# Optimization experiments

Hardware: AMD Instinct MI355X
Metric: run time of the kernel (lower is better)

## Reference

```python
import math
import jax, jax.numpy as jnp
import numpy as np

N_HEADS = 8
FACTOR = 1


def setup_inputs() -> dict:
    key = jax.random.key(0)
    ks = jax.random.split(key, 8)
    B, L, D = 8, 2048, 512
    scale = 0.05
    return {
        "queries": jax.random.normal(ks[0], (B, L, D), jnp.float32),
        "keys": jax.random.normal(ks[1], (B, L, D), jnp.float32),
        "values": jax.random.normal(ks[2], (B, L, D), jnp.float32),
        "Wq": jax.random.normal(ks[3], (D, D), jnp.float32) * scale,
        "bq": jnp.zeros((D,), jnp.float32),
        "Wk": jax.random.normal(ks[4], (D, D), jnp.float32) * scale,
        "bk": jnp.zeros((D,), jnp.float32),
        "Wv": jax.random.normal(ks[5], (D, D), jnp.float32) * scale,
        "bv": jnp.zeros((D,), jnp.float32),
        "Wo": jax.random.normal(ks[6], (D, D), jnp.float32) * scale,
        "bo": jnp.zeros((D,), jnp.float32),
    }


def _autocorrelation(q, k, v):
    # q,k,v: [B, L, H, E]; L == S assumed (as built in setup_inputs)
    B, L, H, E = q.shape
    qp = jnp.transpose(q, (0, 2, 3, 1))  # [B,H,E,L]
    kp = jnp.transpose(k, (0, 2, 3, 1))
    vp = jnp.transpose(v, (0, 2, 3, 1))
    q_fft = jnp.fft.rfft(qp, axis=-1)
    k_fft = jnp.fft.rfft(kp, axis=-1)
    corr = jnp.fft.irfft(q_fft * jnp.conj(k_fft), n=L, axis=-1)  # [B,H,E,L]

    # training-path time-delay aggregation
    top_k = int(FACTOR * math.log(L))  # static python int
    mean_value = corr.mean(axis=(1, 2))  # [B, L]
    _, index = jax.lax.top_k(mean_value.mean(axis=0), top_k)  # [K] global delays
    weights = mean_value[:, index]  # [B, K]
    tmp_corr = jax.nn.softmax(weights, axis=-1)  # [B, K]
    # roll(v, -d) along last axis == gather at (t + d) mod L
    idx = (jnp.arange(L)[None, :] + index[:, None]) % L  # [K, L]
    patterns = vp[..., idx]  # [B,H,E,K,L]
    delays_agg = jnp.einsum('bhekl,bk->bhel', patterns, tmp_corr)  # [B,H,E,L]
    return jnp.transpose(delays_agg, (0, 3, 1, 2))  # [B,L,H,E]


def reference(queries, keys, values, Wq, bq, Wk, bk, Wv, bv, Wo, bo):
    B, L, Dm = queries.shape
    H = N_HEADS
    q = (queries @ Wq + bq).reshape(B, L, H, -1)
    k = (keys @ Wk + bk).reshape(B, L, H, -1)
    v = (values @ Wv + bv).reshape(B, L, H, -1)
    out = _autocorrelation(q, k, v).reshape(B, L, -1)
    return out @ Wo + bo
```

## Files before the change

kernel.cpp:

```cpp
#include <hip/hip_runtime.h>
#include <stdint.h>

#define BATCH 8
#define L_SEQ 2048
#define D_MODEL 512
#define TOPK 7
#define BM 128
#define BN 128
#define BK 32
#define LT 136

typedef _Float16 f16x8 __attribute__((ext_vector_type(8)));
typedef __attribute__((ext_vector_type(4))) float f32x4;
typedef unsigned short u16;
typedef unsigned int u32;

__device__ __forceinline__ u16 f2h(float f) {
    union { _Float16 h; u16 u; } v; v.h = (_Float16)f; return v.u;
}

__device__ __forceinline__ void load_lds16(const u16* g, u16* l) {
    __builtin_amdgcn_global_load_lds(
        (const __attribute__((address_space(1))) u32*)(g),
        (__attribute__((address_space(3))) u32*)(l), 16, 0, 0);
}


__global__ __launch_bounds__(256, 3) void gemm_qkv(
    const float* __restrict__ Xq, const float* __restrict__ Xk, const float* __restrict__ Xv,
    const u16* __restrict__ Wqt, const u16* __restrict__ Wkt, const u16* __restrict__ Wvt,
    const float* __restrict__ bq, const float* __restrict__ bk, const float* __restrict__ bv,
    u16* __restrict__ QT, u16* __restrict__ KT, u16* __restrict__ Vout)
{
    __shared__ __align__(16) u16 smem[2 * BM * 32 + 2 * BN * BK];
    u16* lT = smem;
    u16* lBb = smem + 2 * BM * 32;

    const int tid = threadIdx.x;
    const int hw = blockIdx.x;
    const int lg = (hw & 7) * 192 + (hw >> 3);
    const int bn = lg & 3, bm = (lg >> 2) & 127, z = lg >> 9;

    const int lane = tid & 63, wave = tid >> 6;
    const int wm = wave >> 1, wn = wave & 1;
    const int l15 = lane & 15, quad = lane >> 4;

    const float* A  = (z == 0) ? Xq  : (z == 1) ? Xk  : Xv;
    const u16*   Bt = (z == 0) ? Wqt : (z == 1) ? Wkt : Wvt;
    const float* bias = (z == 0) ? bq : (z == 1) ? bk : bv;

    const int s0 = wave * 64 + lane, s1 = s0 + 256;
    const int r0 = s0 >> 2, c0 = (s0 & 3) ^ ((r0 >> 1) & 3);
    const int r1 = s1 >> 2, c1 = (s1 & 3) ^ ((r1 >> 1) & 3);
    const u16* gB0 = Bt + (long)(bn * BN + r0) * D_MODEL + c0 * 8;
    const u16* gB1 = Bt + (long)(bn * BN + r1) * D_MODEL + c1 * 8;

    int rowj[4], csj[4];
    const float* gA[4];
    #pragma unroll
    for (int j = 0; j < 4; ++j) {
        int idx = tid + j * 256;
        int row = idx >> 3, c4 = (idx & 7) * 4;
        rowj[j] = row;
        csj[j] = (((c4 >> 3) ^ (row & 3)) << 3) | (c4 & 7);
        gA[j] = A + (long)(bm * BM + row) * D_MODEL + c4;
    }

    f32x4 acc[4][4] = {};
    float4 vaA[4];

    {
        load_lds16(gB0, lBb + wave * 512);
        load_lds16(gB1, lBb + 2048 + wave * 512);
        gB0 += BK; gB1 += BK;
        #pragma unroll
        for (int j = 0; j < 4; ++j) {
            float4 va = *(const float4*)(gA[j]);
            ushort4 pa;
            pa.x = f2h(va.x); pa.y = f2h(va.y); pa.z = f2h(va.z); pa.w = f2h(va.w);
            *(ushort4*)&smem[rowj[j] * 32 + csj[j]] = pa;
        }
        #pragma unroll
        for (int j = 0; j < 4; ++j)
            vaA[j] = *(const float4*)(gA[j] + BK);
    }
    __syncthreads();

    #define QKV_FRAGS_MFMA(lAc_, lBc_)                                              \
        {                                                                           \
            f16x8 fa[4], fb[4];                                                     \
            _Pragma("unroll")                                                       \
            for (int i = 0; i < 4; ++i) {                                           \
                int r = wm * 64 + i * 16 + l15;                                     \
                fa[i] = *(const f16x8*)&(lAc_)[r * 32 + ((quad ^ (r & 3)) << 3)];   \
            }                                                                       \
            _Pragma("unroll")                                                       \
            for (int j = 0; j < 4; ++j) {                                           \
                int n = wn * 64 + j * 16 + l15;                                     \
                int cs = quad ^ ((n >> 1) & 3);                                     \
                fb[j] = *(const f16x8*)&(lBc_)[n * 32 + cs * 8];                    \
            }                                                                       \
            _Pragma("unroll")                                                       \
            for (int i = 0; i < 4; ++i)                                             \
                _Pragma("unroll")                                                   \
                for (int j = 0; j < 4; ++j)                                         \
                    acc[i][j] = __builtin_amdgcn_mfma_f32_16x16x32_f16(             \
                        fa[i], fb[j], acc[i][j], 0, 0, 0);                          \
        }

    for (int t = 0; t < 14; ++t) {
        const int cur = t & 1;
        u16* lAc = smem + cur * (BM * 32);
        u16* lBc = lBb + cur * (BN * BK);
        u16* lAn = smem + (cur ^ 1) * (BM * 32);
        u16* lBn = lBb + (cur ^ 1) * (BN * BK);

        #pragma unroll
        for (int j = 0; j < 4; ++j) {
            ushort4 pa;
            pa.x = f2h(vaA[j].x); pa.y = f2h(vaA[j].y);
            pa.z = f2h(vaA[j].z); pa.w = f2h(vaA[j].w);
            *(ushort4*)&lAn[rowj[j] * 32 + csj[j]] = pa;
        }
        __builtin_amdgcn_sched_barrier(0);
        load_lds16(gB0, lBn + wave * 512);
        load_lds16(gB1, lBn + 2048 + wave * 512);
        gB0 += BK; gB1 += BK;
        __builtin_amdgcn_sched_barrier(0);
        #pragma unroll
        for (int j = 0; j < 4; ++j)
            vaA[j] = *(const float4*)(gA[j] + (t + 2) * BK);

        QKV_FRAGS_MFMA(lAc, lBc)

        asm volatile("s_waitcnt vmcnt(4) lgkmcnt(0)" ::: "memory");
        __builtin_amdgcn_sched_barrier(0);
        __builtin_amdgcn_s_barrier();
        __builtin_amdgcn_sched_barrier(0);
    }

    {
        u16* lAc = smem;
        u16* lBc = lBb;
        u16* lAn = smem + BM * 32;
        u16* lBn = lBb + BN * BK;
        #pragma unroll
        for (int j = 0; j < 4; ++j) {
            ushort4 pa;
            pa.x = f2h(vaA[j].x); pa.y = f2h(vaA[j].y);
            pa.z = f2h(vaA[j].z); pa.w = f2h(vaA[j].w);
            *(ushort4*)&lAn[rowj[j] * 32 + csj[j]] = pa;
        }
        __builtin_amdgcn_sched_barrier(0);
        load_lds16(gB0, lBn + wave * 512);
        load_lds16(gB1, lBn + 2048 + wave * 512);

        QKV_FRAGS_MFMA(lAc, lBc)

        asm volatile("s_waitcnt vmcnt(0) lgkmcnt(0)" ::: "memory");
        __builtin_amdgcn_sched_barrier(0);
        __builtin_amdgcn_s_barrier();
        __builtin_amdgcn_sched_barrier(0);
    }

    {
        u16* lAc = smem + BM * 32;
        u16* lBc = lBb + BN * BK;
        QKV_FRAGS_MFMA(lAc, lBc)
    }
    #undef QKV_FRAGS_MFMA

    if (z < 2) {
        u16* out = (z == 0) ? QT : KT;
        const int t0 = (bm * BM) & (L_SEQ - 1);
        const int bb = (bm * BM) >> 11;
        #pragma unroll
        for (int h = 0; h < 2; ++h) {
            __syncthreads();
            if (wn == h) {
                #pragma unroll
                for (int j = 0; j < 4; ++j) {
                    int dloc = j * 16 + l15;
                    float bvv = bias[bn * BN + h * 64 + dloc];
                    #pragma unroll
                    for (int i = 0; i < 4; ++i) {
                        int trow = wm * 64 + i * 16 + quad * 4;
                        #pragma unroll
                        for (int r = 0; r < 4; ++r)
                            lT[dloc * LT + trow + r] = f2h(acc[i][j][r] + bvv);
                    }
                }
            }
            __syncthreads();
            int dloc = tid >> 2, q4 = tid & 3;
            long base = ((long)(bb * D_MODEL + bn * BN + h * 64 + dloc)) * L_SEQ + t0;
            #pragma unroll
            for (int s = 0; s < 4; ++s) {
                int c = q4 * 4 + s;
                *(uint4*)(out + base + c * 8) = *(const uint4*)&lT[dloc * LT + c * 8];
            }
        }
    } else {
        #pragma unroll
        for (int i = 0; i < 4; ++i) {
            int row = bm * BM + wm * 64 + i * 16 + quad * 4;
            #pragma unroll
            for (int j = 0; j < 4; ++j) {
                int col = bn * BN + wn * 64 + j * 16 + l15;
                float bvv = bias[col];
                #pragma unroll
                for (int r = 0; r < 4; ++r)
                    Vout[(long)(row + r) * D_MODEL + col] = f2h(acc[i][j][r] + bvv);
            }
        }
    }
}

__global__ __launch_bounds__(256, 3) void gemm_out_fused(
    const u16* __restrict__ V, const u16* __restrict__ Bt,
    const int* __restrict__ selIdx, const float* __restrict__ selW,
    const float* __restrict__ bias, float* __restrict__ Cp)
{
    __shared__ __align__(16) u16 lA[2 * BM * 32];
    __shared__ __align__(16) u16 lB[2 * BN * BK];

    const int tid = threadIdx.x;
    const int hw = blockIdx.x;
    const int lg = (hw & 7) * 64 + (hw >> 3);
    const int bn = lg & 3, bm = lg >> 2;

    const int lane = tid & 63, wave = tid >> 6;
    const int wm = wave >> 1, wn = wave & 1;
    const int l15 = lane & 15, quad = lane >> 4;

    int sik[TOPK];
    #pragma unroll
    for (int k = 0; k < TOPK; ++k) sik[k] = selIdx[k];

    const int s0 = wave * 64 + lane, s1 = s0 + 256;
    const int r0 = s0 >> 2, c0 = (s0 & 3) ^ ((r0 >> 1) & 3);
    const int r1 = s1 >> 2, c1 = (s1 & 3) ^ ((r1 >> 1) & 3);
    const u16* gB0 = Bt + (long)(bn * BN + r0) * D_MODEL + c0 * 8;
    const u16* gB1 = Bt + (long)(bn * BN + r1) * D_MODEL + c1 * 8;

    const int row_a = tid >> 2,          c8_a = (tid & 3) * 8;
    const int row_b = (tid + 256) >> 2,  c8_b = (tid & 3) * 8;
    const int csa = ((c8_a >> 3) ^ (row_a & 3)) << 3;
    const int csb = ((c8_b >> 3) ^ (row_b & 3)) << 3;
    const int gra = bm * BM + row_a, grb = bm * BM + row_b;
    const int ba = gra >> 11, la = gra & (L_SEQ - 1);
    const int bb = grb >> 11, lb = grb & (L_SEQ - 1);

    _Float16 swa[TOPK], swb[TOPK];
    #pragma unroll
    for (int k = 0; k < TOPK; ++k) {
        swa[k] = (_Float16)selW[ba * TOPK + k];
        swb[k] = (_Float16)selW[bb * TOPK + k];
    }

    union U8 { uint4 u; f16x8 h8; };

    f32x4 acc[4][4] = {};

    {
        load_lds16(gB0, lB + wave * 512);
        load_lds16(gB1, lB + 2048 + wave * 512);
        gB0 += BK; gB1 += BK;
        {
            f16x8 a = {};
            #pragma unroll
            for (int k = 0; k < TOPK; ++k) {
                int src = (la + sik[k]) & (L_SEQ - 1);
                U8 x; x.u = *(const uint4*)(V + ((long)ba * L_SEQ + src) * D_MODEL + c8_a);
                a += x.h8 * swa[k];
            }
            U8 o; o.h8 = a;
            *(uint4*)&lA[row_a * 32 + csa] = o.u;
        }
        {
            f16x8 a = {};
            #pragma unroll
            for (int k = 0; k < TOPK; ++k) {
                int src = (lb + sik[k]) & (L_SEQ - 1);
                U8 x; x.u = *(const uint4*)(V + ((long)bb * L_SEQ + src) * D_MODEL + c8_b);
                a += x.h8 * swb[k];
            }
            U8 o; o.h8 = a;
            *(uint4*)&lA[row_b * 32 + csb] = o.u;
        }
    }
    __syncthreads();

    for (int t = 0; t < 16; ++t) {
        const int cur = t & 1;
        u16* lAc = lA + cur * (BM * 32);
        u16* lBc = lB + cur * (BN * BK);
        u16* lAn = lA + (cur ^ 1) * (BM * 32);
        u16* lBn = lB + (cur ^ 1) * (BN * BK);
        const bool nx = (t < 15);
        const int k1 = (t + 1) * BK;

        U8 xv[7];
        if (nx) {
            load_lds16(gB0, lBn + wave * 512);
            load_lds16(gB1, lBn + 2048 + wave * 512);
            gB0 += BK; gB1 += BK;
            #pragma unroll
            for (int k = 0; k < TOPK; ++k) {
                int src = (la + sik[k]) & (L_SEQ - 1);
                xv[k].u = *(const uint4*)(V + ((long)ba * L_SEQ + src) * D_MODEL + k1 + c8_a);
            }
        }

        f16x8 fa[4], fb[4];
        #pragma unroll
        for (int i = 0; i < 4; ++i) {
            int r = wm * 64 + i * 16 + l15;
            fa[i] = *(const f16x8*)&lAc[r * 32 + ((quad ^ (r & 3)) << 3)];
        }
        #pragma unroll
        for (int j = 0; j < 4; ++j) {
            int n = wn * 64 + j * 16 + l15;
            int cs = quad ^ ((n >> 1) & 3);
            fb[j] = *(const f16x8*)&lBc[n * 32 + cs * 8];
        }

        #pragma unroll
        for (int i = 0; i < 2; ++i)
            #pragma unroll
            for (int j = 0; j < 4; ++j)
                acc[i][j] = __builtin_amdgcn_mfma_f32_16x16x32_f16(fa[i], fb[j], acc[i][j], 0, 0, 0);

        U8 xw[7];
        if (nx) {
            f16x8 a = {};
            #pragma unroll
            for (int k = 0; k < TOPK; ++k) a += xv[k].h8 * swa[k];
            U8 o; o.h8 = a;
            *(uint4*)&lAn[row_a * 32 + csa] = o.u;
            #pragma unroll
            for (int k = 0; k < TOPK; ++k) {
                int src = (lb + sik[k]) & (L_SEQ - 1);
                xw[k].u = *(const uint4*)(V + ((long)bb * L_SEQ + src) * D_MODEL + k1 + c8_b);
            }
        }

        #pragma unroll
        for (int i = 2; i < 4; ++i)
            #pragma unroll
            for (int j = 0; j < 4; ++j)
                acc[i][j] = __builtin_amdgcn_mfma_f32_16x16x32_f16(fa[i], fb[j], acc[i][j], 0, 0, 0);

        if (nx) {
            f16x8 a = {};
            #pragma unroll
            for (int k = 0; k < TOPK; ++k) a += xw[k].h8 * swb[k];
            U8 o; o.h8 = a;
            *(uint4*)&lAn[row_b * 32 + csb] = o.u;
        }
        __syncthreads();
    }

    #pragma unroll
    for (int i = 0; i < 4; ++i) {
        int row = bm * BM + wm * 64 + i * 16 + quad * 4;
        #pragma unroll
        for (int j = 0; j < 4; ++j) {
            int col = bn * BN + wn * 64 + j * 16 + l15;
            float bvv = bias[col];
            #pragma unroll
            for (int r = 0; r < 4; ++r)
                Cp[(long)(row + r) * D_MODEL + col] = acc[i][j][r] + bvv;
        }
    }
}

__device__ __forceinline__ void fft2048_lds2(
    float2* Z, const float2* Tw, int tid)
{
    #pragma unroll
    for (int s = 0; s < 10; s += 2) {
        #pragma unroll
        for (int u = 0; u < 2; ++u) {
            int idx = tid + u * 256;
            int d1 = 1 << s;
            int pos = idx & (d1 - 1);
            int i0 = ((idx >> s) << (s + 2)) + pos;
            float2 w1 = Tw[pos << (10 - s)];
            float2 w2 = Tw[pos << (9 - s)];
            float2 w3 = Tw[(pos + d1) << (9 - s)];
            float2 a = Z[i0];
            float2 b = Z[i0 + d1];
            float2 c = Z[i0 + 2 * d1];
            float2 d = Z[i0 + 3 * d1];
            float t1r = b.x * w1.x - b.y * w1.y, t1i = b.x * w1.y + b.y * w1.x;
            float Ar = a.x + t1r, Ai = a.y + t1i, Br = a.x - t1r, Bi = a.y - t1i;
            float t2r = d.x * w1.x - d.y * w1.y, t2i = d.x * w1.y + d.y * w1.x;
            float Cr = c.x + t2r, Ci = c.y + t2i, Dr = c.x - t2r, Di = c.y - t2i;
            float u1r = Cr * w2.x - Ci * w2.y, u1i = Cr * w2.y + Ci * w2.x;
            float u2r = Dr * w3.x - Di * w3.y, u2i = Dr * w3.y + Di * w3.x;
            float2 o;
            o.x = Ar + u1r; o.y = Ai + u1i; Z[i0]          = o;
            o.x = Ar - u1r; o.y = Ai - u1i; Z[i0 + 2 * d1] = o;
            o.x = Br + u2r; o.y = Bi + u2i; Z[i0 + d1]     = o;
            o.x = Br - u2r; o.y = Bi - u2i; Z[i0 + 3 * d1] = o;
        }
        __syncthreads();
    }
    #pragma unroll
    for (int j = 0; j < 4; ++j) {
        int idx = tid + j * 256;
        float2 w = Tw[idx];
        float2 a = Z[idx], b = Z[idx + 1024];
        float tr = b.x * w.x - b.y * w.y, ti = b.x * w.y + b.y * w.x;
        float2 o;
        o.x = a.x + tr; o.y = a.y + ti; Z[idx] = o;
        o.x = a.x - tr; o.y = a.y - ti; Z[idx + 1024] = o;
    }
    __syncthreads();
}

__global__ __launch_bounds__(256) void fft_corr_fwd(
    const u16* __restrict__ QT, const u16* __restrict__ KT, float* __restrict__ S)
{
    __shared__ float2 Z[2048];
    __shared__ float2 Tw[1024];
    const int tid = threadIdx.x;
    const int b = blockIdx.x >> 7, dg = blockIdx.x & 127;

    #pragma unroll
    for (int j = 0; j < 4; ++j) {
        int i = tid + j * 256;
        float ang = -6.28318530717958647692f * (float)i * (1.0f / 2048.0f);
        float sn, cs; __sincosf(ang, &sn, &cs);
        float2 w; w.x = cs; w.y = sn;
        Tw[i] = w;
    }

    float sr[8] = {0,0,0,0,0,0,0,0};
    float si8[8] = {0,0,0,0,0,0,0,0};

    for (int g = 0; g < 4; ++g) {
        int d = dg * 4 + g;
        const u16* qrow = QT + ((long)b * D_MODEL + d) * L_SEQ;
        const u16* krow = KT + ((long)b * D_MODEL + d) * L_SEQ;
        __syncthreads();
        union { uint4 u; _Float16 h[8]; } xq, xk;
        xq.u = *(const uint4*)(qrow + tid * 8);
        xk.u = *(const uint4*)(krow + tid * 8);
        #pragma unroll
        for (int j = 0; j < 8; ++j) {
            int t = tid * 8 + j;
            int tr = (int)(__brev((unsigned)t) >> 21);
            float2 z; z.x = (float)xq.h[j]; z.y = (float)xk.h[j];
            Z[tr] = z;
        }
        __syncthreads();
        fft2048_lds2(Z, Tw, tid);
        #pragma unroll
        for (int j = 0; j < 8; ++j) {
            int f = tid + j * 256;
            int fm = (2048 - f) & 2047;
            float2 X = Z[f], Xm = Z[fm];
            float qr = 0.5f * (X.x + Xm.x), qi = 0.5f * (X.y - Xm.y);
            float dr = X.x - Xm.x,          di = X.y + Xm.y;
            float kr = 0.5f * di,           ki = -0.5f * dr;
            sr[j]  += qr * kr + qi * ki;
            si8[j] += qi * kr - qr * ki;
        }
    }
    #pragma unroll
    for (int j = 0; j < 8; ++j) {
        int f = tid + j * 256;
        atomicAdd(&S[((long)b * 2048 + f) * 2 + 0], sr[j]);
        atomicAdd(&S[((long)b * 2048 + f) * 2 + 1], si8[j]);
    }
}

__global__ __launch_bounds__(256) void fft_corr_inv(
    const float* __restrict__ S, float* __restrict__ raw)
{
    __shared__ float2 Z[2048];
    __shared__ float2 Tw[1024];
    const int tid = threadIdx.x;
    const int b = blockIdx.x;

    #pragma unroll
    for (int j = 0; j < 4; ++j) {
        int i = tid + j * 256;
        float ang = 6.28318530717958647692f * (float)i * (1.0f / 2048.0f);
        float sn, cs; __sincosf(ang, &sn, &cs);
        float2 w; w.x = cs; w.y = sn;
        Tw[i] = w;
    }
    #pragma unroll
    for (int j = 0; j < 8; ++j) {
        int f = tid + j * 256;
        int fr = (int)(__brev((unsigned)f) >> 21);
        Z[fr] = *(const float2*)(S + ((long)b * 2048 + f) * 2);
    }
    __syncthreads();
    fft2048_lds2(Z, Tw, tid);
    #pragma unroll
    for (int j = 0; j < 8; ++j) {
        int t = tid + j * 256;
        raw[(long)b * 2048 + t] = Z[t].x * (1.0f / 2048.0f);
    }
}

__global__ __launch_bounds__(256) void transposeW4(
    const float* __restrict__ Wq, const float* __restrict__ Wk,
    const float* __restrict__ Wv, const float* __restrict__ Wo, u16* __restrict__ dstBase)
{
    __shared__ float t[32][33];
    const int z = blockIdx.z;
    const float* src = (z == 0) ? Wq : (z == 1) ? Wk : (z == 2) ? Wv : Wo;
    u16* dst = dstBase + (long)z * D_MODEL * D_MODEL;
    int tx = threadIdx.x & 31, ty = threadIdx.x >> 5;
    int c0 = blockIdx.x * 32, r0 = blockIdx.y * 32;
    #pragma unroll
    for (int r = ty; r < 32; r += 8)
        t[r][tx] = src[(long)(r0 + r) * D_MODEL + c0 + tx];
    __syncthreads();
    #pragma unroll
    for (int r = ty; r < 32; r += 8)
        dst[(long)(c0 + r) * D_MODEL + r0 + tx] = f2h(t[tx][r]);
}

__global__ __launch_bounds__(256) void select_topk(
    const float* __restrict__ raw, int* __restrict__ selIdx, float* __restrict__ selW)
{
    __shared__ float g[L_SEQ];
    __shared__ float wv[4];
    __shared__ int   wi[4];
    __shared__ int   sidx[TOPK];
    __shared__ float wbuf[BATCH][TOPK];
    int tid = threadIdx.x;
    int lane = tid & 63, wave = tid >> 6;
    for (int t = tid; t < L_SEQ; t += 256) {
        float s = 0.0f;
        #pragma unroll
        for (int b = 0; b < BATCH; ++b) s += raw[b * L_SEQ + t];
        g[t] = s;
    }
    __syncthreads();
    for (int it = 0; it < TOPK; ++it) {
        float best = -1e30f; int bi = 0x7fffffff;
        #pragma unroll
        for (int j = 0; j < 8; ++j) {
            int t = tid + j * 256;
            float v = g[t];
            if (v > best || (v == best && t < bi)) { best = v; bi = t; }
        }
        #pragma unroll
        for (int s = 32; s > 0; s >>= 1) {
            float v2 = __shfl_xor(best, s);
            int   i2 = __shfl_xor(bi, s);
            if (v2 > best || (v2 == best && i2 < bi)) { best = v2; bi = i2; }
        }
        if (lane == 0) { wv[wave] = best; wi[wave] = bi; }
        __syncthreads();
        if (tid == 0) {
            float b0 = wv[0]; int i0 = wi[0];
            #pragma unroll
            for (int w = 1; w < 4; ++w)
                if (wv[w] > b0 || (wv[w] == b0 && wi[w] < i0)) { b0 = wv[w]; i0 = wi[w]; }
            sidx[it] = i0; g[i0] = -1e30f;
        }
        __syncthreads();
    }
    if (tid < BATCH * TOPK) {
        int b = tid / TOPK, k = tid % TOPK;
        wbuf[b][k] = raw[b * L_SEQ + sidx[k]] * (1.0f / 512.0f);
    }
    __syncthreads();
    if (tid < BATCH) {
        float mx = -1e30f;
        #pragma unroll
        for (int k = 0; k < TOPK; ++k) mx = fmaxf(mx, wbuf[tid][k]);
        float e[TOPK]; float sum = 0.0f;
        #pragma unroll
        for (int k = 0; k < TOPK; ++k) { e[k] = expf(wbuf[tid][k] - mx); sum += e[k]; }
        #pragma unroll
        for (int k = 0; k < TOPK; ++k) selW[tid * TOPK + k] = e[k] / sum;
    }
    if (tid < TOPK) selIdx[tid] = sidx[tid];
}

extern "C" void kernel_launch(void* const* d_in, const int* in_sizes, int n_in,
                              void* d_out, int out_size, void* d_ws, size_t ws_size,
                              hipStream_t stream)
{
    (void)in_sizes; (void)n_in; (void)out_size; (void)ws_size;
    const float* Xq = (const float*)d_in[0];
    const float* Xk = (const float*)d_in[1];
    const float* Xv = (const float*)d_in[2];
    const float* Wq = (const float*)d_in[3];
    const float* bq = (const float*)d_in[4];
    const float* Wk = (const float*)d_in[5];
    const float* bk = (const float*)d_in[6];
    const float* Wv = (const float*)d_in[7];
    const float* bv = (const float*)d_in[8];
    const float* Wo = (const float*)d_in[9];
    const float* bo = (const float*)d_in[10];

    char* ws = (char*)d_ws;
    const long SLABH = (long)BATCH * L_SEQ * D_MODEL * sizeof(u16);
    u16* QT   = (u16*)(ws);
    u16* KT   = (u16*)(ws + SLABH);
    u16* Vf   = (u16*)(ws + 2 * SLABH);
    const long WSZ = (long)D_MODEL * D_MODEL;
    u16* Wt   = (u16*)(ws + 3 * SLABH);
    u16* Wqt = Wt + 0 * WSZ; u16* Wkt = Wt + 1 * WSZ;
    u16* Wvt = Wt + 2 * WSZ; u16* Wot = Wt + 3 * WSZ;
    float* S   = (float*)(ws + 3 * SLABH + 4 * WSZ * sizeof(u16));
    float* raw = S + (long)BATCH * L_SEQ * 2;
    int*   sIdx = (int*)(raw + (long)BATCH * L_SEQ);
    float* sW   = (float*)(sIdx + 8);

    dim3 tb(256);
    transposeW4<<<dim3(16, 16, 4), tb, 0, stream>>>(Wq, Wk, Wv, Wo, Wt);
    hipMemsetAsync(S, 0, (long)BATCH * L_SEQ * 2 * sizeof(float), stream);

    gemm_qkv<<<dim3(1536), tb, 0, stream>>>(Xq, Xk, Xv, Wqt, Wkt, Wvt, bq, bk, bv, QT, KT, Vf);

    fft_corr_fwd<<<dim3(1024), tb, 0, stream>>>(QT, KT, S);
    fft_corr_inv<<<dim3(BATCH), tb, 0, stream>>>(S, raw);
    select_topk<<<1, tb, 0, stream>>>(raw, sIdx, sW);

    gemm_out_fused<<<dim3(512), tb, 0, stream>>>(Vf, Wot, sIdx, sW, bo, (float*)d_out);
}
```

Baseline: 311.0 us.

## Fuse inverse FFT with top-k selection using linearity and direct DFT for weights

Sums the per-batch spectra before a single inverse FFT, relying on linearity, so one block computes the batch-summed correlation instead of eight separate inverse FFTs. The same block then runs the top-k selection and evaluates each batch's correlation at the chosen delays with a direct DFT sum over the spectrum, removing the separate select_topk launch and the raw buffer. The memset of S is folded into the weight-transpose kernel, so one fewer API call is made. The cost is that the fused stage runs as one serial block doing extra DFT work, where the inverse FFTs previously ran across eight blocks.

```diff
diff --git a/kernel.cpp b/kernel.cpp
--- a/kernel.cpp
+++ b/kernel.cpp
@@ -477,13 +477,19 @@
     }
 }
 
-__global__ __launch_bounds__(256) void fft_corr_inv(
-    const float* __restrict__ S, float* __restrict__ raw)
+__global__ __launch_bounds__(256) void fft_inv_topk(
+    const float* __restrict__ S, int* __restrict__ selIdx, float* __restrict__ selW)
 {
     __shared__ float2 Z[2048];
     __shared__ float2 Tw[1024];
+    __shared__ float g[L_SEQ];
+    __shared__ float wv[4];
+    __shared__ int   wi[4];
+    __shared__ int   sidx[TOPK];
+    __shared__ float wbuf[BATCH][TOPK];
+
     const int tid = threadIdx.x;
-    const int b = blockIdx.x;
+    const int lane = tid & 63, wave = tid >> 6;
 
     #pragma unroll
     for (int j = 0; j < 4; ++j) {
@@ -497,20 +503,89 @@
     for (int j = 0; j < 8; ++j) {
         int f = tid + j * 256;
         int fr = (int)(__brev((unsigned)f) >> 21);
-        Z[fr] = *(const float2*)(S + ((long)b * 2048 + f) * 2);
+        float sx = 0.f, sy = 0.f;
+        #pragma unroll
+        for (int b = 0; b < BATCH; ++b) {
+            float2 v = *(const float2*)(S + ((long)b * 2048 + f) * 2);
+            sx += v.x; sy += v.y;
+        }
+        float2 z; z.x = sx; z.y = sy;
+        Z[fr] = z;
     }
     __syncthreads();
     fft2048_lds2(Z, Tw, tid);
     #pragma unroll
     for (int j = 0; j < 8; ++j) {
         int t = tid + j * 256;
-        raw[(long)b * 2048 + t] = Z[t].x * (1.0f / 2048.0f);
-    }
+        g[t] = Z[t].x * (1.0f / 2048.0f);
+    }
+    __syncthreads();
+
+    for (int it = 0; it < TOPK; ++it) {
+        float best = -1e30f; int bi = 0x7fffffff;
+        #pragma unroll
+        for (int j = 0; j < 8; ++j) {
+            int t = tid + j * 256;
+            float v = g[t];
+            if (v > best || (v == best && t < bi)) { best = v; bi = t; }
+        }
+        #pragma unroll
+        for (int s = 32; s > 0; s >>= 1) {
+            float v2 = __shfl_xor(best, s);
+            int   i2 = __shfl_xor(bi, s);
+            if (v2 > best || (v2 == best && i2 < bi)) { best = v2; bi = i2; }
+        }
+        if (lane == 0) { wv[wave] = best; wi[wave] = bi; }
+        __syncthreads();
+        if (tid == 0) {
+            float b0 = wv[0]; int i0 = wi[0];
+            #pragma unroll
+            for (int w = 1; w < 4; ++w)
+                if (wv[w] > b0 || (wv[w] == b0 && wi[w] < i0)) { b0 = wv[w]; i0 = wi[w]; }
+            sidx[it] = i0; g[i0] = -1e30f;
+        }
+        __syncthreads();
+    }
+
+    #pragma unroll
+    for (int h = 0; h < 2; ++h) {
+        int b = wave + h * 4;
+        #pragma unroll
+        for (int k = 0; k < TOPK; ++k) {
+            int idx = sidx[k];
+            float part = 0.f;
+            for (int i = 0; i < 32; ++i) {
+                int f = lane + i * 64;
+                int m = (f * idx) & 2047;
+                float2 w2 = Tw[m & 1023];
+                float2 sv = *(const float2*)(S + ((long)b * 2048 + f) * 2);
+                float re = sv.x * w2.x - sv.y * w2.y;
+                part += (m & 1024) ? -re : re;
+            }
+            #pragma unroll
+            for (int s = 32; s > 0; s >>= 1) part += __shfl_xor(part, s);
+            if (lane == 0) wbuf[b][k] = part * (1.0f / 2048.0f) * (1.0f / 512.0f);
+        }
+    }
+    __syncthreads();
+
+    if (tid < BATCH) {
+        float mx = -1e30f;
+        #pragma unroll
+        for (int k = 0; k < TOPK; ++k) mx = fmaxf(mx, wbuf[tid][k]);
+        float e[TOPK]; float sum = 0.0f;
+        #pragma unroll
+        for (int k = 0; k < TOPK; ++k) { e[k] = expf(wbuf[tid][k] - mx); sum += e[k]; }
+        #pragma unroll
+        for (int k = 0; k < TOPK; ++k) selW[tid * TOPK + k] = e[k] / sum;
+    }
+    if (tid < TOPK) selIdx[tid] = sidx[tid];
 }
 
 __global__ __launch_bounds__(256) void transposeW4(
     const float* __restrict__ Wq, const float* __restrict__ Wk,
-    const float* __restrict__ Wv, const float* __restrict__ Wo, u16* __restrict__ dstBase)
+    const float* __restrict__ Wv, const float* __restrict__ Wo, u16* __restrict__ dstBase,
+    float* __restrict__ Sz)
 {
     __shared__ float t[32][33];
     const int z = blockIdx.z;
@@ -518,6 +593,10 @@
     u16* dst = dstBase + (long)z * D_MODEL * D_MODEL;
     int tx = threadIdx.x & 31, ty = threadIdx.x >> 5;
     int c0 = blockIdx.x * 32, r0 = blockIdx.y * 32;
+
+    const int fb = (blockIdx.z * 16 + blockIdx.y) * 16 + blockIdx.x;
+    if (threadIdx.x < 32) Sz[fb * 32 + threadIdx.x] = 0.0f;
+
     #pragma unroll
     for (int r = ty; r < 32; r += 8)
         t[r][tx] = src[(long)(r0 + r) * D_MODEL + c0 + tx];
@@ -525,66 +604,6 @@
     #pragma unroll
     for (int r = ty; r < 32; r += 8)
         dst[(long)(c0 + r) * D_MODEL + r0 + tx] = f2h(t[tx][r]);
-}
-
-__global__ __launch_bounds__(256) void select_topk(
-    const float* __restrict__ raw, int* __restrict__ selIdx, float* __restrict__ selW)
-{
-    __shared__ float g[L_SEQ];
-    __shared__ float wv[4];
-    __shared__ int   wi[4];
-    __shared__ int   sidx[TOPK];
-    __shared__ float wbuf[BATCH][TOPK];
-    int tid = threadIdx.x;
-    int lane = tid & 63, wave = tid >> 6;
-    for (int t = tid; t < L_SEQ; t += 256) {
-        float s = 0.0f;
-        #pragma unroll
-        for (int b = 0; b < BATCH; ++b) s += raw[b * L_SEQ + t];
-        g[t] = s;
-    }
-    __syncthreads();
-    for (int it = 0; it < TOPK; ++it) {
-        float best = -1e30f; int bi = 0x7fffffff;
-        #pragma unroll
-        for (int j = 0; j < 8; ++j) {
-            int t = tid + j * 256;
-            float v = g[t];
-            if (v > best || (v == best && t < bi)) { best = v; bi = t; }
-        }
-        #pragma unroll
-        for (int s = 32; s > 0; s >>= 1) {
-            float v2 = __shfl_xor(best, s);
-            int   i2 = __shfl_xor(bi, s);
-            if (v2 > best || (v2 == best && i2 < bi)) { best = v2; bi = i2; }
-        }
-        if (lane == 0) { wv[wave] = best; wi[wave] = bi; }
-        __syncthreads();
-        if (tid == 0) {
-            float b0 = wv[0]; int i0 = wi[0];
-            #pragma unroll
-            for (int w = 1; w < 4; ++w)
-                if (wv[w] > b0 || (wv[w] == b0 && wi[w] < i0)) { b0 = wv[w]; i0 = wi[w]; }
-            sidx[it] = i0; g[i0] = -1e30f;
-        }
-        __syncthreads();
-    }
-    if (tid < BATCH * TOPK) {
-        int b = tid / TOPK, k = tid % TOPK;
-        wbuf[b][k] = raw[b * L_SEQ + sidx[k]] * (1.0f / 512.0f);
-    }
-    __syncthreads();
-    if (tid < BATCH) {
-        float mx = -1e30f;
-        #pragma unroll
-        for (int k = 0; k < TOPK; ++k) mx = fmaxf(mx, wbuf[tid][k]);
-        float e[TOPK]; float sum = 0.0f;
-        #pragma unroll
-        for (int k = 0; k < TOPK; ++k) { e[k] = expf(wbuf[tid][k] - mx); sum += e[k]; }
-        #pragma unroll
-        for (int k = 0; k < TOPK; ++k) selW[tid * TOPK + k] = e[k] / sum;
-    }
-    if (tid < TOPK) selIdx[tid] = sidx[tid];
 }
 
 extern "C" void kernel_launch(void* const* d_in, const int* in_sizes, int n_in,
@@ -614,19 +633,16 @@
     u16* Wqt = Wt + 0 * WSZ; u16* Wkt = Wt + 1 * WSZ;
     u16* Wvt = Wt + 2 * WSZ; u16* Wot = Wt + 3 * WSZ;
     float* S   = (float*)(ws + 3 * SLABH + 4 * WSZ * sizeof(u16));
-    float* raw = S + (long)BATCH * L_SEQ * 2;
-    int*   sIdx = (int*)(raw + (long)BATCH * L_SEQ);
+    int*   sIdx = (int*)(S + (long)BATCH * L_SEQ * 2);
     float* sW   = (float*)(sIdx + 8);
 
     dim3 tb(256);
-    transposeW4<<<dim3(16, 16, 4), tb, 0, stream>>>(Wq, Wk, Wv, Wo, Wt);
-    hipMemsetAsync(S, 0, (long)BATCH * L_SEQ * 2 * sizeof(float), stream);
+    transposeW4<<<dim3(16, 16, 4), tb, 0, stream>>>(Wq, Wk, Wv, Wo, Wt, S);
 
     gemm_qkv<<<dim3(1536), tb, 0, stream>>>(Xq, Xk, Xv, Wqt, Wkt, Wvt, bq, bk, bv, QT, KT, Vf);
 
     fft_corr_fwd<<<dim3(1024), tb, 0, stream>>>(QT, KT, S);
-    fft_corr_inv<<<dim3(BATCH), tb, 0, stream>>>(S, raw);
-    select_topk<<<1, tb, 0, stream>>>(raw, sIdx, sW);
+    fft_inv_topk<<<dim3(1), tb, 0, stream>>>(S, sIdx, sW);
 
     gemm_out_fused<<<dim3(512), tb, 0, stream>>>(Vf, Wot, sIdx, sW, bo, (float*)d_out);
 }
```

After: 343.5 us. 10.4% more time.
